# Kernel tuning notes

Hardware: AMD Instinct MI355X
Metric: run time of the kernel (lower is better)

Reference implementation:

```python
import jax, jax.numpy as jnp
import numpy as np

EPS = 1e-10
BETA = 0.25


def setup_inputs() -> dict:
    key = jax.random.key(0)
    k1, k2 = jax.random.split(key)
    z = jax.random.normal(k1, (32, 256, 32, 32), dtype=jnp.float32)
    # codebook initialized uniform(-1/K, 1/K) in the original; scale doesn't affect math shape
    K = 1024
    codebook = jax.random.uniform(k2, (K, 256), dtype=jnp.float32,
                                  minval=-1.0 / K, maxval=1.0 / K)
    return {"z": z, "codebook": codebook}


def reference(z, codebook):
    b, d, h, w = z.shape
    K = codebook.shape[0]
    # (b d h w) -> (b h w, d)
    z_flat = jnp.transpose(z, (0, 2, 3, 1)).reshape(-1, d)  # [N, d]
    N = z_flat.shape[0]

    # squared L2 distances: ||z||^2 + ||c||^2 - 2 z.c  -> [N, K]
    distances = (jnp.sum(z_flat ** 2, axis=1, keepdims=True)
                 + jnp.sum(codebook ** 2, axis=1)
                 - 2.0 * jnp.einsum('nd,kd->nk', z_flat, codebook))

    encoding_indices = jnp.argmin(distances, axis=1)  # [N]

    # codebook usage histogram == mean of one-hot encodings over N
    encodings_mean = jnp.zeros((K,), dtype=z.dtype).at[encoding_indices].add(1.0) / N
    perplexity = jnp.exp(-jnp.sum(encodings_mean * jnp.log(encodings_mean + EPS)))

    zq_flat = codebook[encoding_indices]  # [N, d]
    z_quantized = jnp.transpose(zq_flat.reshape(b, h, w, d), (0, 3, 1, 2))

    mse = jnp.mean((z_quantized - z) ** 2)
    loss = BETA * mse + mse  # encoder + codebook terms are numerically equal in fwd

    quantized_st = z + jax.lax.stop_gradient(z_quantized - z)
    return (quantized_st, loss, perplexity, encoding_indices, distances)
```

## Files before the change

### kernel.cpp

```cpp
#include <hip/hip_runtime.h>
#include <hip/hip_bf16.h>
#include <math.h>

constexpr int D = 256;
constexpr int N = 32768;
constexpr int K = 1024;
constexpr float MARGIN = 1.5e-3f;

constexpr int OFF_Q    = 0;
constexpr int OFF_LOSS = 8388608;
constexpr int OFF_PERP = 8388609;
constexpr int OFF_IDX  = 8388610;
constexpr int OFF_DIST = 8421378;

using f32x4 = __attribute__((ext_vector_type(4))) float;
using s16x8 = __attribute__((ext_vector_type(8))) short;
using u16x8 = __attribute__((ext_vector_type(8))) unsigned short;
using u16x4 = __attribute__((ext_vector_type(4))) unsigned short;

#define GLOAD_LDS16(g, l)                                                     \
    __builtin_amdgcn_global_load_lds(                                         \
        (const __attribute__((address_space(1))) void*)(g),                   \
        (__attribute__((address_space(3))) void*)(l), 16, 0, 0)

__device__ __forceinline__ unsigned short bf16_bits(float v) {
    __hip_bfloat16 h = __float2bfloat16(v);
    return *(unsigned short*)&h;
}

__global__ __launch_bounds__(256) void split_z_kernel(const float* __restrict__ z,
                                                      unsigned short* __restrict__ A,
                                                      float* __restrict__ z_t,
                                                      float* __restrict__ znorm) {
    __shared__ float tile[64][65];
    __shared__ float znp[64][4];
    int t = threadIdx.x;
    int r0 = blockIdx.x * 64;
    int b  = blockIdx.y;
    const float* zb = z + (size_t)b * D * 1024;
    int rr4 = (t & 15) * 4;
    int rr = t >> 2, chunk = t & 3;
    size_t n = (size_t)b * 1024 + r0 + rr;
    float zacc = 0.f;

    for (int dblk = 0; dblk < 4; ++dblk) {
        int d0 = dblk * 64;
        if (dblk) __syncthreads();
        #pragma unroll
        for (int i = 0; i < 4; ++i) {
            int di = i * 16 + (t >> 4);
            float4 v = *(const float4*)(zb + (size_t)(d0 + di) * 1024 + r0 + rr4);
            *(float4*)&tile[di][rr4] = v;
        }
        __syncthreads();

        unsigned short hbuf[16];
        float fbuf[16];
        #pragma unroll
        for (int i = 0; i < 16; ++i) {
            float v = tile[chunk * 16 + i][rr];
            fbuf[i] = v;
            hbuf[i] = bf16_bits(v);
            zacc += v * v;
        }
        unsigned short* pa = A + n * 256 + d0 + chunk * 16;
        *(u16x8*)(pa + 0) = *(u16x8*)&hbuf[0];
        *(u16x8*)(pa + 8) = *(u16x8*)&hbuf[8];
        float* pz = z_t + n * 256 + d0 + chunk * 16;
        #pragma unroll
        for (int q = 0; q < 4; ++q)
            *(float4*)(pz + q * 4) = *(float4*)&fbuf[q * 4];
    }
    znp[rr][chunk] = zacc;
    __syncthreads();
    if (t < 64) {
        float s = znp[t][0] + znp[t][1] + znp[t][2] + znp[t][3];
        znorm[(size_t)b * 1024 + r0 + t] = s;
    }
}

__global__ __launch_bounds__(256) void split_cb_kernel(const float* __restrict__ cb,
                                                       unsigned short* __restrict__ Bb,
                                                       float* __restrict__ cnorm,
                                                       int* __restrict__ hist) {
    int gid = blockIdx.x * 256 + threadIdx.x;
    if (gid < K) hist[gid] = 0;
    int k = blockIdx.x * 4 + (threadIdx.x >> 6);
    int lane = threadIdx.x & 63;
    float4 v = *(const float4*)(cb + (size_t)k * D + lane * 4);
    unsigned short hb[4] = {bf16_bits(v.x), bf16_bits(v.y), bf16_bits(v.z), bf16_bits(v.w)};
    *(u16x4*)(Bb + (size_t)k * 256 + lane * 4) = *(u16x4*)&hb[0];
    float s = v.x * v.x + v.y * v.y + v.z * v.z + v.w * v.w;
    #pragma unroll
    for (int off = 32; off; off >>= 1) s += __shfl_down(s, off, 64);
    if (lane == 0) cnorm[k] = s;
}

__global__ __launch_bounds__(256) void dist_gemm_mfma(const unsigned short* __restrict__ A,
                                                      const unsigned short* __restrict__ Bb,
                                                      const float* __restrict__ znorm,
                                                      const float* __restrict__ cnorm,
                                                      float* __restrict__ dist,
                                                      float* __restrict__ pmin,
                                                      unsigned long long* __restrict__ pmask) {
    __shared__ unsigned short As[128 * 64];
    __shared__ unsigned short Bs[128 * 64];

    int t = threadIdx.x;
    int l = t & 63;
    int w = t >> 6;
    int p = blockIdx.x;
    int xcd = p & 7, j = p >> 3;
    int nb = xcd * 32 + (j >> 3);
    int kbl = j & 7;
    int k0 = kbl * 128;
    int n0 = nb * 128;

    int srow = t >> 3;
    int scol = (t & 7) * 8;
    const unsigned short* Ab = A + ((size_t)(n0 + srow)) * 256 + scol;
    const unsigned short* Bbp = Bb + ((size_t)(k0 + srow)) * 256 + scol;
    unsigned short* AsBase = As + t * 8;
    unsigned short* BsBase = Bs + t * 8;

    f32x4 acc[4][4];
    #pragma unroll
    for (int i = 0; i < 4; ++i)
        #pragma unroll
        for (int jj = 0; jj < 4; ++jj) acc[i][jj] = (f32x4){0.f, 0.f, 0.f, 0.f};

    int wr = w >> 1, wc = w & 1;
    int aRowBase = wr * 64 + (l & 15);
    int bRowBase = wc * 64 + (l & 15);
    int kLane = (l >> 4) * 8;

    #pragma unroll
    for (int kt = 0; kt < 4; ++kt) {
        int col = kt * 64;
        #pragma unroll
        for (int pass = 0; pass < 4; ++pass) {
            GLOAD_LDS16(Ab + (size_t)pass * 32 * 256 + col, AsBase + pass * 2048);
            GLOAD_LDS16(Bbp + (size_t)pass * 32 * 256 + col, BsBase + pass * 2048);
        }
        __syncthreads();

        #pragma unroll
        for (int kk = 0; kk < 64; kk += 32) {
            s16x8 af[4], bf[4];
            #pragma unroll
            for (int mf = 0; mf < 4; ++mf)
                af[mf] = *(const s16x8*)&As[(aRowBase + mf * 16) * 64 + kk + kLane];
            #pragma unroll
            for (int nf = 0; nf < 4; ++nf)
                bf[nf] = *(const s16x8*)&Bs[(bRowBase + nf * 16) * 64 + kk + kLane];
            #pragma unroll
            for (int mf = 0; mf < 4; ++mf)
                #pragma unroll
                for (int nf = 0; nf < 4; ++nf)
                    acc[mf][nf] = __builtin_amdgcn_mfma_f32_16x16x32_bf16(
                        af[mf], bf[nf], acc[mf][nf], 0, 0, 0);
        }
        if (kt < 3) __syncthreads();
    }

    int colBase = k0 + wc * 64 + (l & 15);
    int rowBase = n0 + wr * 64 + (l >> 4) * 4;
    int kb = kbl * 2 + wc;
    int g = l >> 4;
    float cn[4];
    #pragma unroll
    for (int nf = 0; nf < 4; ++nf) cn[nf] = cnorm[colBase + nf * 16];
    #pragma unroll
    for (int mf = 0; mf < 4; ++mf) {
        #pragma unroll
        for (int r = 0; r < 4; ++r) {
            int n = rowBase + mf * 16 + r;
            float zn = znorm[n];
            float* pr = dist + (size_t)n * K;
            float dv[4];
            #pragma unroll
            for (int nf = 0; nf < 4; ++nf) {
                dv[nf] = zn + cn[nf] - 2.0f * acc[mf][nf][r];
                pr[colBase + nf * 16] = dv[nf];
            }
            float m4 = fminf(fminf(dv[0], dv[1]), fminf(dv[2], dv[3]));
            #pragma unroll
            for (int off = 1; off < 16; off <<= 1)
                m4 = fminf(m4, __shfl_xor(m4, off, 64));
            float th = m4 + MARGIN;
            unsigned long long bal[4];
            #pragma unroll
            for (int nf = 0; nf < 4; ++nf)
                bal[nf] = __ballot(dv[nf] <= th);
            if ((l & 15) == 0) {
                unsigned long long msk = 0;
                #pragma unroll
                for (int nf = 0; nf < 4; ++nf)
                    msk |= ((bal[nf] >> (g * 16)) & 0xFFFFULL) << (nf * 16);
                pmin[(size_t)n * 16 + kb] = m4;
                pmask[(size_t)n * 16 + kb] = msk;
            }
        }
    }
}

__global__ __launch_bounds__(256) void resolve_kernel(const float* __restrict__ pmin,
                                                      const unsigned long long* __restrict__ pmask,
                                                      const float* __restrict__ z_t,
                                                      const float* __restrict__ cb,
                                                      const float* __restrict__ znorm,
                                                      const float* __restrict__ cnorm,
                                                      int* __restrict__ idx_i,
                                                      float* __restrict__ out_idx,
                                                      int* __restrict__ hist) {
    int n = blockIdx.x * 4 + (threadIdx.x >> 6);
    int lane = threadIdx.x & 63;
    int s16 = lane & 15;

    float myp = pmin[(size_t)n * 16 + s16];
    float gmin = myp;
    #pragma unroll
    for (int off = 1; off < 16; off <<= 1)
        gmin = fminf(gmin, __shfl_xor(gmin, off, 64));
    float th = gmin + MARGIN;

    unsigned long long mym = (myp <= th) ? pmask[(size_t)n * 16 + s16] : 0ULL;
    int mycnt = __popcll(mym);
    int total = mycnt;
    #pragma unroll
    for (int off = 1; off < 16; off <<= 1)
        total += __shfl_xor(total, off, 64);

    int besti;
    if (total == 1) {
        int cand = mym ? (s16 * 64 + __builtin_ctzll(mym)) : 0x7fffffff;
        #pragma unroll
        for (int off = 1; off < 16; off <<= 1)
            cand = min(cand, __shfl_xor(cand, off, 64));
        besti = cand;
    } else {
        float4 zr = *(const float4*)(z_t + (size_t)n * 256 + lane * 4);
        float zn = znorm[n];
        float bestv = INFINITY;
        besti = 0x7fffffff;
        for (int kb = 0; kb < 16; ++kb) {
            unsigned long long m = __shfl(mym, kb, 64);
            while (m) {
                int lb = __builtin_ctzll(m);
                m &= m - 1;
                int k = kb * 64 + lb;
                float4 cr = *(const float4*)(cb + (size_t)k * D + lane * 4);
                float s = zr.x * cr.x + zr.y * cr.y + zr.z * cr.z + zr.w * cr.w;
                #pragma unroll
                for (int off = 1; off < 64; off <<= 1)
                    s += __shfl_xor(s, off, 64);
                float dd = zn + cnorm[k] - 2.0f * s;
                if (dd < bestv) { bestv = dd; besti = k; }
            }
        }
    }

    if (lane == 0) {
        idx_i[n] = besti;
        out_idx[n] = (float)besti;
        atomicAdd(&hist[besti], 1);
    }
}

__global__ __launch_bounds__(256) void gather_kernel(const float* __restrict__ z,
                                                     const float* __restrict__ cb,
                                                     const int* __restrict__ idx_i,
                                                     float* __restrict__ out_q,
                                                     float* __restrict__ mse_partial) {
    int n = blockIdx.x * 256 + threadIdx.x;
    int b = n >> 10, r = n & 1023;
    const float* zp = z + (size_t)b * D * 1024 + r;
    float* qp = out_q + (size_t)b * D * 1024 + r;
    const float* crow = cb + (size_t)idx_i[n] * D;

    float s = 0.f;
    for (int c = 0; c < D; c += 4) {
        float4 zq4 = *(const float4*)(crow + c);
        float zq[4] = {zq4.x, zq4.y, zq4.z, zq4.w};
        #pragma unroll
        for (int m = 0; m < 4; ++m) {
            float zv = zp[(size_t)(c + m) * 1024];
            float d = zq[m] - zv;
            qp[(size_t)(c + m) * 1024] = zv + d;
            s += d * d;
        }
    }
    __shared__ float red[256];
    red[threadIdx.x] = s;
    __syncthreads();
    #pragma unroll
    for (int off = 128; off; off >>= 1) {
        if (threadIdx.x < off) red[threadIdx.x] += red[threadIdx.x + off];
        __syncthreads();
    }
    if (threadIdx.x == 0) mse_partial[blockIdx.x] = red[0];
}

__global__ __launch_bounds__(1024) void finalize_kernel(const int* __restrict__ hist,
                                                        const float* __restrict__ mse_partial,
                                                        float* __restrict__ out) {
    __shared__ float red[1024];
    int t = threadIdx.x;
    float p = (float)hist[t] * (1.0f / (float)N);
    red[t] = p * logf(p + 1e-10f);
    __syncthreads();
    #pragma unroll
    for (int off = 512; off; off >>= 1) {
        if (t < off) red[t] += red[t + off];
        __syncthreads();
    }
    float ent = red[0];
    __syncthreads();
    red[t] = (t < 128) ? mse_partial[t] : 0.f;
    __syncthreads();
    #pragma unroll
    for (int off = 512; off; off >>= 1) {
        if (t < off) red[t] += red[t + off];
        __syncthreads();
    }
    if (t == 0) {
        float mse = red[0] / (float)((size_t)N * D);
        out[OFF_LOSS] = 1.25f * mse;
        out[OFF_PERP] = expf(-ent);
    }
}

extern "C" void kernel_launch(void* const* d_in, const int* in_sizes, int n_in,
                              void* d_out, int out_size, void* d_ws, size_t ws_size,
                              hipStream_t stream) {
    const float* z  = (const float*)d_in[0];
    const float* cb = (const float*)d_in[1];
    float* out = (float*)d_out;

    char* wsb = (char*)d_ws;
    size_t off = 0;
    unsigned short* A  = (unsigned short*)(wsb + off); off += (size_t)N * 256 * 2;
    float* z_t         = (float*)(wsb + off);          off += (size_t)N * 256 * 4;
    unsigned short* Bb = (unsigned short*)(wsb + off); off += (size_t)K * 256 * 2;
    float* pmin        = (float*)(wsb + off);          off += (size_t)N * 16 * 4;
    unsigned long long* pmask = (unsigned long long*)(wsb + off); off += (size_t)N * 16 * 8;
    float* znorm       = (float*)(wsb + off);          off += (size_t)N * 4;
    float* cnorm       = (float*)(wsb + off);          off += (size_t)K * 4;
    float* mse_partial = (float*)(wsb + off);          off += 128 * 4;
    int* hist          = (int*)(wsb + off);            off += (size_t)K * 4;
    int* idx_i         = (int*)(wsb + off);

    split_z_kernel<<<dim3(16, 32), 256, 0, stream>>>(z, A, z_t, znorm);
    split_cb_kernel<<<K / 4, 256, 0, stream>>>(cb, Bb, cnorm, hist);
    dist_gemm_mfma<<<2048, 256, 0, stream>>>(A, Bb, znorm, cnorm,
                                             out + OFF_DIST, pmin, pmask);
    resolve_kernel<<<N / 4, 256, 0, stream>>>(pmin, pmask, z_t, cb, znorm, cnorm,
                                              idx_i, out + OFF_IDX, hist);
    gather_kernel<<<N / 256, 256, 0, stream>>>(z, cb, idx_i, out + OFF_Q, mse_partial);
    finalize_kernel<<<1, 1024, 0, stream>>>(hist, mse_partial, out);
}
```

Measured before the change: 114.3 us.

## Derive MSE from min distances, drop z reread in gather, fuse small kernels

The loss MSE is now computed by summing each row's minimum distance in resolve_kernel, since the quantization error equals the chosen squared distance. The gather kernel therefore no longer reads z and simply writes codebook rows into the transposed output. Gather is spread over 8 column slices for more parallelism. The codebook conversion is folded into split_z as an extra block row, and finalize is folded into one gather block, removing two launches. The risk is accuracy: the MSE now uses the approximate bf16 GEMM minimum rather than the exact float difference, and the straight-through output is written as zq instead of z+(zq-z).

```diff
diff --git a/kernel.cpp b/kernel.cpp
--- a/kernel.cpp
+++ b/kernel.cpp
@@ -29,12 +29,35 @@
 }
 
 __global__ __launch_bounds__(256) void split_z_kernel(const float* __restrict__ z,
+                                                      const float* __restrict__ cb,
                                                       unsigned short* __restrict__ A,
                                                       float* __restrict__ z_t,
-                                                      float* __restrict__ znorm) {
+                                                      float* __restrict__ znorm,
+                                                      unsigned short* __restrict__ Bb,
+                                                      float* __restrict__ cnorm,
+                                                      int* __restrict__ hist) {
+    int t = threadIdx.x;
+    if (blockIdx.y == 32) {
+        int gid = blockIdx.x * 256 + t;
+        if (gid < K) hist[gid] = 0;
+        int lane = t & 63, wv = t >> 6;
+        #pragma unroll 4
+        for (int i = 0; i < 16; ++i) {
+            int k = blockIdx.x * 64 + wv * 16 + i;
+            float4 v = *(const float4*)(cb + (size_t)k * D + lane * 4);
+            unsigned short hb[4] = {bf16_bits(v.x), bf16_bits(v.y),
+                                    bf16_bits(v.z), bf16_bits(v.w)};
+            *(u16x4*)(Bb + (size_t)k * D + lane * 4) = *(u16x4*)&hb[0];
+            float s = v.x * v.x + v.y * v.y + v.z * v.z + v.w * v.w;
+            #pragma unroll
+            for (int off = 32; off; off >>= 1) s += __shfl_down(s, off, 64);
+            if (lane == 0) cnorm[k] = s;
+        }
+        return;
+    }
+
     __shared__ float tile[64][65];
     __shared__ float znp[64][4];
-    int t = threadIdx.x;
     int r0 = blockIdx.x * 64;
     int b  = blockIdx.y;
     const float* zb = z + (size_t)b * D * 1024;
@@ -77,23 +100,6 @@
         float s = znp[t][0] + znp[t][1] + znp[t][2] + znp[t][3];
         znorm[(size_t)b * 1024 + r0 + t] = s;
     }
-}
-
-__global__ __launch_bounds__(256) void split_cb_kernel(const float* __restrict__ cb,
-                                                       unsigned short* __restrict__ Bb,
-                                                       float* __restrict__ cnorm,
-                                                       int* __restrict__ hist) {
-    int gid = blockIdx.x * 256 + threadIdx.x;
-    if (gid < K) hist[gid] = 0;
-    int k = blockIdx.x * 4 + (threadIdx.x >> 6);
-    int lane = threadIdx.x & 63;
-    float4 v = *(const float4*)(cb + (size_t)k * D + lane * 4);
-    unsigned short hb[4] = {bf16_bits(v.x), bf16_bits(v.y), bf16_bits(v.z), bf16_bits(v.w)};
-    *(u16x4*)(Bb + (size_t)k * 256 + lane * 4) = *(u16x4*)&hb[0];
-    float s = v.x * v.x + v.y * v.y + v.z * v.z + v.w * v.w;
-    #pragma unroll
-    for (int off = 32; off; off >>= 1) s += __shfl_down(s, off, 64);
-    if (lane == 0) cnorm[k] = s;
 }
 
 __global__ __launch_bounds__(256) void dist_gemm_mfma(const unsigned short* __restrict__ A,
@@ -212,7 +218,9 @@
                                                       const float* __restrict__ cnorm,
                                                       int* __restrict__ idx_i,
                                                       float* __restrict__ out_idx,
-                                                      int* __restrict__ hist) {
+                                                      int* __restrict__ hist,
+                                                      float* __restrict__ mse_part) {
+    __shared__ float s4[4];
     int n = blockIdx.x * 4 + (threadIdx.x >> 6);
     int lane = threadIdx.x & 63;
     int s16 = lane & 15;
@@ -225,8 +233,7 @@
     float th = gmin + MARGIN;
 
     unsigned long long mym = (myp <= th) ? pmask[(size_t)n * 16 + s16] : 0ULL;
-    int mycnt = __popcll(mym);
-    int total = mycnt;
+    int total = __popcll(mym);
     #pragma unroll
     for (int off = 1; off < 16; off <<= 1)
         total += __shfl_xor(total, off, 64);
@@ -264,69 +271,65 @@
         idx_i[n] = besti;
         out_idx[n] = (float)besti;
         atomicAdd(&hist[besti], 1);
-    }
-}
-
-__global__ __launch_bounds__(256) void gather_kernel(const float* __restrict__ z,
-                                                     const float* __restrict__ cb,
+        s4[threadIdx.x >> 6] = gmin;
+    }
+    __syncthreads();
+    if (threadIdx.x == 0)
+        mse_part[blockIdx.x] = (s4[0] + s4[1]) + (s4[2] + s4[3]);
+}
+
+__global__ __launch_bounds__(256) void gather_kernel(const float* __restrict__ cb,
                                                      const int* __restrict__ idx_i,
                                                      float* __restrict__ out_q,
-                                                     float* __restrict__ mse_partial) {
-    int n = blockIdx.x * 256 + threadIdx.x;
+                                                     const float* __restrict__ mse_part,
+                                                     const int* __restrict__ hist,
+                                                     float* __restrict__ out) {
+    int t = threadIdx.x;
+    int n = blockIdx.x * 256 + t;
     int b = n >> 10, r = n & 1023;
-    const float* zp = z + (size_t)b * D * 1024 + r;
     float* qp = out_q + (size_t)b * D * 1024 + r;
     const float* crow = cb + (size_t)idx_i[n] * D;
-
-    float s = 0.f;
-    for (int c = 0; c < D; c += 4) {
-        float4 zq4 = *(const float4*)(crow + c);
-        float zq[4] = {zq4.x, zq4.y, zq4.z, zq4.w};
-        #pragma unroll
-        for (int m = 0; m < 4; ++m) {
-            float zv = zp[(size_t)(c + m) * 1024];
-            float d = zq[m] - zv;
-            qp[(size_t)(c + m) * 1024] = zv + d;
-            s += d * d;
-        }
-    }
-    __shared__ float red[256];
-    red[threadIdx.x] = s;
-    __syncthreads();
-    #pragma unroll
-    for (int off = 128; off; off >>= 1) {
-        if (threadIdx.x < off) red[threadIdx.x] += red[threadIdx.x + off];
-        __syncthreads();
-    }
-    if (threadIdx.x == 0) mse_partial[blockIdx.x] = red[0];
-}
-
-__global__ __launch_bounds__(1024) void finalize_kernel(const int* __restrict__ hist,
-                                                        const float* __restrict__ mse_partial,
-                                                        float* __restrict__ out) {
-    __shared__ float red[1024];
-    int t = threadIdx.x;
-    float p = (float)hist[t] * (1.0f / (float)N);
-    red[t] = p * logf(p + 1e-10f);
-    __syncthreads();
-    #pragma unroll
-    for (int off = 512; off; off >>= 1) {
-        if (t < off) red[t] += red[t + off];
-        __syncthreads();
-    }
-    float ent = red[0];
-    __syncthreads();
-    red[t] = (t < 128) ? mse_partial[t] : 0.f;
-    __syncthreads();
-    #pragma unroll
-    for (int off = 512; off; off >>= 1) {
-        if (t < off) red[t] += red[t + off];
-        __syncthreads();
-    }
-    if (t == 0) {
-        float mse = red[0] / (float)((size_t)N * D);
-        out[OFF_LOSS] = 1.25f * mse;
-        out[OFF_PERP] = expf(-ent);
+    int c0 = blockIdx.y * 32;
+
+    #pragma unroll
+    for (int c = 0; c < 32; c += 4) {
+        float4 v = *(const float4*)(crow + c0 + c);
+        qp[(size_t)(c0 + c + 0) * 1024] = v.x;
+        qp[(size_t)(c0 + c + 1) * 1024] = v.y;
+        qp[(size_t)(c0 + c + 2) * 1024] = v.z;
+        qp[(size_t)(c0 + c + 3) * 1024] = v.w;
+    }
+
+    if (blockIdx.x == 0 && blockIdx.y == 0) {
+        __shared__ float red[256];
+        float s = 0.f;
+        for (int i = t; i < 8192; i += 256) s += mse_part[i];
+        red[t] = s;
+        __syncthreads();
+        #pragma unroll
+        for (int off = 128; off; off >>= 1) {
+            if (t < off) red[t] += red[t + off];
+            __syncthreads();
+        }
+        float msesum = red[0];
+        __syncthreads();
+        float e = 0.f;
+        for (int k = t; k < K; k += 256) {
+            float p = (float)hist[k] * (1.0f / (float)N);
+            e += p * logf(p + 1e-10f);
+        }
+        red[t] = e;
+        __syncthreads();
+        #pragma unroll
+        for (int off = 128; off; off >>= 1) {
+            if (t < off) red[t] += red[t + off];
+            __syncthreads();
+        }
+        if (t == 0) {
+            float mse = msesum / (float)((size_t)N * D);
+            out[OFF_LOSS] = 1.25f * mse;
+            out[OFF_PERP] = expf(-red[0]);
+        }
     }
 }
 
@@ -346,16 +349,15 @@
     unsigned long long* pmask = (unsigned long long*)(wsb + off); off += (size_t)N * 16 * 8;
     float* znorm       = (float*)(wsb + off);          off += (size_t)N * 4;
     float* cnorm       = (float*)(wsb + off);          off += (size_t)K * 4;
-    float* mse_partial = (float*)(wsb + off);          off += 128 * 4;
+    float* mse_part    = (float*)(wsb + off);          off += 8192 * 4;
     int* hist          = (int*)(wsb + off);            off += (size_t)K * 4;
     int* idx_i         = (int*)(wsb + off);
 
-    split_z_kernel<<<dim3(16, 32), 256, 0, stream>>>(z, A, z_t, znorm);
-    split_cb_kernel<<<K / 4, 256, 0, stream>>>(cb, Bb, cnorm, hist);
+    split_z_kernel<<<dim3(16, 33), 256, 0, stream>>>(z, cb, A, z_t, znorm, Bb, cnorm, hist);
     dist_gemm_mfma<<<2048, 256, 0, stream>>>(A, Bb, znorm, cnorm,
                                              out + OFF_DIST, pmin, pmask);
     resolve_kernel<<<N / 4, 256, 0, stream>>>(pmin, pmask, z_t, cb, znorm, cnorm,
-                                              idx_i, out + OFF_IDX, hist);
-    gather_kernel<<<N / 256, 256, 0, stream>>>(z, cb, idx_i, out + OFF_Q, mse_partial);
-    finalize_kernel<<<1, 1024, 0, stream>>>(hist, mse_partial, out);
-}
+                                              idx_i, out + OFF_IDX, hist, mse_part);
+    gather_kernel<<<dim3(128, 8), 256, 0, stream>>>(cb, idx_i, out + OFF_Q,
+                                                    mse_part, hist, out);
+}
```

Result: faster. 111.4 us (-2.6%).
